# Kernel optimization log

Measured on AMD Instinct MI355X. Metric: run time of the kernel, lower is better.

## Reference

```python
import jax, jax.numpy as jnp
import numpy as np

N = 1_000_000
E = 1_000_000
K = 512
H = 64
F_IN = 19
N_ITERS = 3
EPS = 1e-5

def _leaky(x):
    return jax.nn.leaky_relu(x, negative_slope=0.01)

def _layernorm(x, g, b):
    mu = jnp.mean(x, axis=-1, keepdims=True)
    var = jnp.var(x, axis=-1, keepdims=True)
    return (x - mu) * jax.lax.rsqrt(var + EPS) * g + b

def setup_inputs() -> dict:
    key = jax.random.key(0)
    ks = jax.random.split(key, 20)
    s = 0.1
    inp = {
        "x": jax.random.normal(ks[0], (N, F_IN), dtype=jnp.float32),
        "edge_index": jax.random.randint(ks[1], (2, E), 0, N, dtype=jnp.int64),
        "candidate_indices": jax.random.randint(ks[2], (K,), 0, N, dtype=jnp.int64),
        # embedding params
        "pW_in": jax.random.normal(ks[3], (F_IN, H), dtype=jnp.float32) * s,
        "pb_in": jnp.zeros((H,), dtype=jnp.float32),
        "eW": jax.random.normal(ks[4], (2, H, H), dtype=jnp.float32) * s,
        "eb": jnp.zeros((2, H), dtype=jnp.float32),
        "gamma": jnp.ones((2, H), dtype=jnp.float32),
        "beta": jnp.zeros((2, H), dtype=jnp.float32),
        # bottom-up step MLPs (stacked over n_iters)
        "sW1": jax.random.normal(ks[5], (N_ITERS, H, H), dtype=jnp.float32) * s,
        "sb1": jnp.zeros((N_ITERS, H), dtype=jnp.float32),
        "sW2": jax.random.normal(ks[6], (N_ITERS, H, H), dtype=jnp.float32) * s,
        "sb2": jnp.zeros((N_ITERS, H), dtype=jnp.float32),
        # score head
        "hW1": jax.random.normal(ks[7], (H, H), dtype=jnp.float32) * s,
        "hb1": jnp.zeros((H,), dtype=jnp.float32),
        "hW2": jax.random.normal(ks[8], (H, 1), dtype=jnp.float32) * s,
        "hb2": jnp.zeros((1,), dtype=jnp.float32),
    }
    return inp

def reference(x, edge_index, candidate_indices, pW_in, pb_in, eW, eb, gamma, beta,
              sW1, sb1, sW2, sb2, hW1, hb1, hW2, hb2):
    # TreeNodeEmbedding: proj + 2 residual layers with LayerNorm
    h = _leaky(x @ pW_in + pb_in)
    for i in range(2):
        h = _layernorm(h + _leaky(h @ eW[i] + eb[i]), gamma[i], beta[i])
    parent_idx = edge_index[0]
    child_idx = edge_index[1]
    # Bottom-up message passing: scatter-mean over children, tiny MLP update
    for i in range(N_ITERS):
        child_h = h[child_idx]                                   # [E, H] gather
        sum_p = jax.ops.segment_sum(child_h, parent_idx, num_segments=N)  # [N, H]
        cnt = jax.ops.segment_sum(jnp.ones((E,), dtype=h.dtype), parent_idx, num_segments=N)  # [N]
        mean_p = sum_p / jnp.maximum(cnt, 1.0)[:, None]
        mask = (cnt > 0)[:, None]
        delta = _leaky(mean_p @ sW1[i] + sb1[i]) @ sW2[i] + sb2[i]
        h = h + jnp.where(mask, delta, 0.0)
    # Score head on candidates, softmax over k (all candidates real -> full_logits == scores)
    cand_h = h[candidate_indices]                                # [K, H]
    scores = (_leaky(cand_h @ hW1 + hb1) @ hW2 + hb2)[:, 0]      # [K]
    probs = jax.nn.softmax(scores)
    return probs
```

## Files before the change

### kernel.cpp

```cpp
#include <hip/hip_runtime.h>
#include <hip/hip_bf16.h>
#include <math.h>

#define H 64
#define FIN 19
#define EPSLN 1e-5f

#define OFF_PW   0
#define OFF_PB   1280
#define OFF_EW   1344
#define OFF_EB   9536
#define OFF_G    9664
#define OFF_BT   9792
#define OFF_W1   9920
#define OFF_W2   22208
#define OFF_B1   34496
#define OFF_B2   34688
#define OFF_HW1  34880
#define OFF_HB1  38976
#define OFF_HW2  39040
#define OFF_HB2  39104
#define WTS_TOTAL 39105

__device__ __forceinline__ float leaky(float v) { return v > 0.f ? v : 0.01f * v; }

__device__ __forceinline__ float wsumf(float v) {
#pragma unroll
  for (int off = 32; off > 0; off >>= 1) v += __shfl_xor(v, off, 64);
  return v;
}

__device__ __forceinline__ bool detect_bf16(const unsigned short* xs) {
  const int lane = threadIdx.x & 63;
  unsigned a = xs[lane], b = xs[64 + lane];
  unsigned ea = (a >> 7) & 0xFFu, ebx = (b >> 7) & 0xFFu;
  return !__any((int)(ea > 140u || ebx > 140u));
}

__device__ __forceinline__ bool detect_i64(const int* w) {
  const int lane = threadIdx.x & 63;
  return __all((int)(w[2 * lane + 1] == 0));
}

__device__ __forceinline__ float ldf(const void* p, size_t i, bool bf) {
  return bf ? __bfloat162float(((const __hip_bfloat16*)p)[i]) : ((const float*)p)[i];
}

struct WT {
  const void* src[14];
  int off[14], len[14], sl[14], rp[14], rs[14], cs[14];
};

__global__ __launch_bounds__(256) void prep_wts(WT T, const unsigned short* xs,
                                                float* wts, int total) {
  const bool bf = detect_bf16(xs);
  for (int i = blockIdx.x * 256 + threadIdx.x; i < total; i += gridDim.x * 256) {
    int p = 0;
    while (i >= T.off[p] + T.len[p]) ++p;
    const int loc = i - T.off[p];
    float v;
    if (T.rp[p] == 0) {
      v = ldf(T.src[p], loc, bf);
    } else {
      const int s = loc / T.sl[p];
      const int r = loc - s * T.sl[p];
      const int j = r / T.rp[p];
      const int k = r - j * T.rp[p];
      v = (k < T.rs[p])
              ? ldf(T.src[p], (size_t)s * T.rs[p] * T.cs[p] + (size_t)k * T.cs[p] + j, bf)
              : 0.f;
    }
    wts[i] = v;
  }
}

__device__ float embed_math(const void* x, const float* wts, float* stg, int v,
                            int lane, bool bf) {
  float xv = (lane < FIN) ? ldf(x, (size_t)v * FIN + lane, bf) : 0.f;
  stg[lane] = xv;
  __syncthreads();
  const float* tp = wts + OFF_PW + lane * 20;
  float a0 = wts[OFF_PB + lane], a1 = 0.f, a2 = 0.f, a3 = 0.f;
#pragma unroll
  for (int k = 0; k < 20; k += 4) {
    float4 m = *(const float4*)&stg[k];
    float4 w = *(const float4*)&tp[k];
    a0 += m.x * w.x; a1 += m.y * w.y; a2 += m.z * w.z; a3 += m.w * w.w;
  }
  __syncthreads();
  float h = leaky((a0 + a1) + (a2 + a3));
#pragma unroll
  for (int L = 0; L < 2; ++L) {
    stg[lane] = h;
    __syncthreads();
    const float* tw = wts + OFF_EW + L * 4096 + lane * 64;
    a0 = wts[OFF_EB + L * 64 + lane]; a1 = a2 = a3 = 0.f;
#pragma unroll
    for (int k = 0; k < H; k += 4) {
      float4 m = *(const float4*)&stg[k];
      float4 w = *(const float4*)&tw[k];
      a0 += m.x * w.x; a1 += m.y * w.y; a2 += m.z * w.z; a3 += m.w * w.w;
    }
    __syncthreads();
    float val = h + leaky((a0 + a1) + (a2 + a3));
    float mu = wsumf(val) * (1.f / 64.f);
    float d = val - mu;
    float var = wsumf(d * d) * (1.f / 64.f);
    h = d * (1.f / sqrtf(var + EPSLN)) * wts[OFF_G + L * 64 + lane] +
        wts[OFF_BT + L * 64 + lane];
  }
  return h;
}

__device__ float delta_math(const float* wts, float* stg, float mean, int it, int lane) {
  stg[lane] = mean;
  __syncthreads();
  const float* w1 = wts + OFF_W1 + it * 4096 + lane * 64;
  float a0 = wts[OFF_B1 + it * 64 + lane], a1 = 0.f, a2 = 0.f, a3 = 0.f;
#pragma unroll
  for (int k = 0; k < H; k += 4) {
    float4 m = *(const float4*)&stg[k];
    float4 w = *(const float4*)&w1[k];
    a0 += m.x * w.x; a1 += m.y * w.y; a2 += m.z * w.z; a3 += m.w * w.w;
  }
  __syncthreads();
  float t1 = leaky((a0 + a1) + (a2 + a3));
  stg[lane] = t1;
  __syncthreads();
  const float* w2 = wts + OFF_W2 + it * 4096 + lane * 64;
  a0 = wts[OFF_B2 + it * 64 + lane]; a1 = a2 = a3 = 0.f;
#pragma unroll
  for (int k = 0; k < H; k += 4) {
    float4 m = *(const float4*)&stg[k];
    float4 w = *(const float4*)&w2[k];
    a0 += m.x * w.x; a1 += m.y * w.y; a2 += m.z * w.z; a3 += m.w * w.w;
  }
  __syncthreads();
  return (a0 + a1) + (a2 + a3);
}

__global__ __launch_bounds__(256) void init_kernel(int* map, int nN, int* counters, int K,
                                                   int* ch3, int n3, int* ch2, int n2,
                                                   int* ch1, int n1) {
  const int tid = blockIdx.x * 256 + threadIdx.x;
  const int stride = gridDim.x * 256;
  for (int i = tid; i < nN; i += stride) map[i] = 0;
  for (int i = tid; i < n3; i += stride) ch3[i] = -1;
  for (int i = tid; i < n2; i += stride) ch2[i] = -1;
  for (int i = tid; i < n1; i += stride) ch1[i] = -1;
  if (tid < 3) counters[tid] = 0;
  if (tid == 3) counters[3] = K;
}

__global__ __launch_bounds__(64) void seed_kernel(const int* cand_raw, int K, int nN,
                                                  int* map, int* node3, int* nextSame3,
                                                  int* selfChild3, int* ctr2, int cap2,
                                                  int* node2) {
  const bool i64 = detect_i64(cand_raw);
  int t = blockIdx.x * 64 + threadIdx.x;
  if (t >= K) return;
  int cv = i64 ? cand_raw[2 * t] : cand_raw[t];
  unsigned n = (unsigned)cv;
  if (n >= (unsigned)nN) n = 0;
  node3[t] = (int)n;
  int enc = (1 << 24) | t;
  int old = atomicExch(&map[n], enc);
  nextSame3[t] = ((old >> 24) == 1) ? (old & 0xFFFFFF) : -1;
  int s = atomicAdd(ctr2, 1);
  if (s < cap2) { node2[s] = (int)n; selfChild3[t] = s; } else selfChild3[t] = 0;
}

__global__ __launch_bounds__(256) void regself_kernel(const int* ctrU_, int capU,
                                                      const int* nodeU, int* map, int epoch,
                                                      int* nextSameU, int* ctrD, int capD,
                                                      int* nodeD, int* selfChildU) {
  int cnt = *ctrU_; if (cnt > capU) cnt = capU;
  int t = blockIdx.x * 256 + threadIdx.x;
  if (t >= cnt) return;
  int n = nodeU[t];
  int enc = (epoch << 24) | t;
  int old = atomicExch(&map[n], enc);
  nextSameU[t] = ((old >> 24) == epoch) ? (old & 0xFFFFFF) : -1;
  int s = atomicAdd(ctrD, 1);
  if (s < capD) { nodeD[s] = n; selfChildU[t] = s; } else selfChildU[t] = 0;
}

__global__ __launch_bounds__(256) void scan_kernel(const int* eraw, int E, int nN,
                                                   const int* map, int epoch,
                                                   const int* nextSameU, int* childHeadU,
                                                   int* ctrD, int capD, int* nodeD,
                                                   int* childNextD) {
  const bool i64 = detect_i64(eraw);
  int e = blockIdx.x * 256 + threadIdx.x;
  if (e >= E) return;
  int pv = i64 ? eraw[2 * e] : eraw[e];
  unsigned p = (unsigned)pv;
  if (p >= (unsigned)nN) p = 0;
  int m = map[p];
  if ((m >> 24) != epoch) return;
  int cv = i64 ? eraw[2 * (E + e)] : eraw[E + e];
  unsigned c = (unsigned)cv;
  if (c >= (unsigned)nN) c = 0;
  int t = m & 0xFFFFFF;
  while (t >= 0) {
    int ct = atomicAdd(ctrD, 1);
    if (ct < capD) {
      nodeD[ct] = (int)c;
      childNextD[ct] = atomicExch(&childHeadU[t], ct);
    }
    t = nextSameU[t];
  }
}

__global__ __launch_bounds__(64) void eval0_kernel(const void* x, const int* ctr0_,
                                                   int cap0, const int* node0,
                                                   const float* wts, float* val0) {
  __shared__ float stg[H];
  int cnt = *ctr0_; if (cnt > cap0) cnt = cap0;
  const int t = blockIdx.x;
  if (t >= cnt) return;
  const int lane = threadIdx.x;
  const bool bf = detect_bf16((const unsigned short*)x);
  float h = embed_math(x, wts, stg, node0[t], lane, bf);
  val0[(size_t)t * H + lane] = h;
}

__global__ __launch_bounds__(64) void evalL_kernel(const int* ctrU_, int capU,
                                                   const int* selfChildU,
                                                   const int* childHeadU,
                                                   const int* childNextD,
                                                   const float* valD, float* valU,
                                                   const float* wts, int it) {
  __shared__ float stg[H];
  int cnt = *ctrU_; if (cnt > capU) cnt = capU;
  const int t = blockIdx.x;
  if (t >= cnt) return;
  const int lane = threadIdx.x;
  float hv = valD[(size_t)selfChildU[t] * H + lane];
  float acc = 0.f;
  int k = 0;
  int c = childHeadU[t];
  while (c >= 0) { acc += valD[(size_t)c * H + lane]; ++k; c = childNextD[c]; }
  if (k > 0) hv += delta_math(wts, stg, acc / (float)k, it, lane);
  valU[(size_t)t * H + lane] = hv;
}

__global__ __launch_bounds__(512) void score_kernel(
    const float* __restrict__ candH, const float* __restrict__ wts,
    const void* x, void* out, int K) {
  __shared__ float red[512];
  const int t = threadIdx.x;
  const bool bf = detect_bf16((const unsigned short*)x);
  float sc = 0.f;
  if (t < K) {
    float hr[H];
#pragma unroll
    for (int k = 0; k < H; k += 4) {
      float4 v = *(const float4*)&candH[(size_t)t * H + k];
      hr[k] = v.x; hr[k + 1] = v.y; hr[k + 2] = v.z; hr[k + 3] = v.w;
    }
    for (int j = 0; j < H; ++j) {
      float a = wts[OFF_HB1 + j];
#pragma unroll
      for (int k = 0; k < H; k += 4) {
        float4 w = *(const float4*)&wts[OFF_HW1 + j * 64 + k];
        a += hr[k] * w.x + hr[k + 1] * w.y + hr[k + 2] * w.z + hr[k + 3] * w.w;
      }
      sc += leaky(a) * wts[OFF_HW2 + j];
    }
    sc += wts[OFF_HB2];
  }
  red[t] = (t < K) ? sc : -3.0e38f;
  __syncthreads();
  for (int off = 256; off > 0; off >>= 1) {
    if (t < off) red[t] = fmaxf(red[t], red[t + off]);
    __syncthreads();
  }
  const float m = red[0];
  __syncthreads();
  const float ex = (t < K) ? expf(sc - m) : 0.f;
  red[t] = ex;
  __syncthreads();
  for (int off = 256; off > 0; off >>= 1) {
    if (t < off) red[t] += red[t + off];
    __syncthreads();
  }
  const float inv = 1.f / red[0];
  if (t < K) {
    float p = ex * inv;
    if (bf) ((__hip_bfloat16*)out)[t] = __float2bfloat16(p);
    else    ((float*)out)[t] = p;
  }
}

extern "C" void kernel_launch(void* const* d_in, const int* in_sizes, int n_in,
                              void* d_out, int out_size, void* d_ws, size_t ws_size,
                              hipStream_t stream) {
  const void* x   = d_in[0];
  const int* edge = (const int*)d_in[1];
  const int* cand = (const int*)d_in[2];
  const int nN = in_sizes[0] / FIN;
  const int E  = in_sizes[1] / 2;
  const int K  = in_sizes[2];

  const int CAP2 = 8 * K, CAP1 = 16 * K, CAP0 = 32 * K;

  auto al = [](size_t b) -> size_t { return (b + 255) & ~(size_t)255; };
  const size_t szW   = (size_t)WTS_TOTAL * sizeof(float);
  const size_t szMap = (size_t)nN * sizeof(int);
  const size_t szK   = (size_t)K * sizeof(int);
  const size_t sz2   = (size_t)CAP2 * sizeof(int);
  const size_t sz1   = (size_t)CAP1 * sizeof(int);
  const size_t sz0   = (size_t)CAP0 * sizeof(int);
  const size_t szV0  = (size_t)CAP0 * H * sizeof(float);
  const size_t szV1  = (size_t)CAP1 * H * sizeof(float);
  const size_t szV2  = (size_t)CAP2 * H * sizeof(float);
  const size_t szV3  = (size_t)K * H * sizeof(float);
  const size_t need = al(szW) + al(szMap) + 256  +
                      4 * al(szK) + 5 * al(sz2) + 5 * al(sz1) + 2 * al(sz0) +
                      al(szV0) + al(szV1) + al(szV2) + al(szV3);

  if (K > 2048 || K < 128 || E < 128 || ws_size < need) return;

  char* wsb = (char*)d_ws;
  size_t off = 0;
  auto carve = [&](size_t bytes) -> void* {
    void* p = wsb + off;
    off += (bytes + 255) & ~(size_t)255;
    return p;
  };
  float* wts     = (float*)carve(szW);
  int* map       = (int*)carve(szMap);
  int* counters  = (int*)carve(256);
  int* node3     = (int*)carve(szK);
  int* nextSame3 = (int*)carve(szK);
  int* selfCh3   = (int*)carve(szK);
  int* chHead3   = (int*)carve(szK);
  int* node2     = (int*)carve(sz2);
  int* nextSame2 = (int*)carve(sz2);
  int* selfCh2   = (int*)carve(sz2);
  int* chHead2   = (int*)carve(sz2);
  int* chNext2   = (int*)carve(sz2);
  int* node1     = (int*)carve(sz1);
  int* nextSame1 = (int*)carve(sz1);
  int* selfCh1   = (int*)carve(sz1);
  int* chHead1   = (int*)carve(sz1);
  int* chNext1   = (int*)carve(sz1);
  int* node0     = (int*)carve(sz0);
  int* chNext0   = (int*)carve(sz0);
  float* val0    = (float*)carve(szV0);
  float* val1    = (float*)carve(szV1);
  float* val2    = (float*)carve(szV2);
  float* val3    = (float*)carve(szV3);

  WT T;
  auto setv = [&](int i, const void* s, int o, int l) {
    T.src[i] = s; T.off[i] = o; T.len[i] = l; T.sl[i] = l;
    T.rp[i] = 0; T.rs[i] = 0; T.cs[i] = 0;
  };
  auto setm = [&](int i, const void* s, int o, int l, int sl, int rpad, int rs, int cs) {
    T.src[i] = s; T.off[i] = o; T.len[i] = l; T.sl[i] = sl;
    T.rp[i] = rpad; T.rs[i] = rs; T.cs[i] = cs;
  };
  setm(0,  d_in[3],  OFF_PW,  1280, 1280, 20, 19, 64);
  setv(1,  d_in[4],  OFF_PB,  64);
  setm(2,  d_in[5],  OFF_EW,  8192, 4096, 64, 64, 64);
  setv(3,  d_in[6],  OFF_EB,  128);
  setv(4,  d_in[7],  OFF_G,   128);
  setv(5,  d_in[8],  OFF_BT,  128);
  setm(6,  d_in[9],  OFF_W1,  12288, 4096, 64, 64, 64);
  setm(7,  d_in[11], OFF_W2,  12288, 4096, 64, 64, 64);
  setv(8,  d_in[10], OFF_B1,  192);
  setv(9,  d_in[12], OFF_B2,  192);
  setm(10, d_in[13], OFF_HW1, 4096, 4096, 64, 64, 64);
  setv(11, d_in[14], OFF_HB1, 64);
  setv(12, d_in[15], OFF_HW2, 64);
  setv(13, d_in[16], OFF_HB2, 1);

  prep_wts<<<160, 256, 0, stream>>>(T, (const unsigned short*)x, wts, WTS_TOTAL);

  init_kernel<<<1024, 256, 0, stream>>>(map, nN, counters, K, chHead3, K,
                                        chHead2, CAP2, chHead1, CAP1);

  seed_kernel<<<(K + 63) / 64, 64, 0, stream>>>(cand, K, nN, map, node3, nextSame3,
                                                selfCh3, &counters[0], CAP2, node2);
  scan_kernel<<<(E + 255) / 256, 256, 0, stream>>>(edge, E, nN, map, 1, nextSame3,
                                                   chHead3, &counters[0], CAP2,
                                                   node2, chNext2);
  regself_kernel<<<(CAP2 + 255) / 256, 256, 0, stream>>>(&counters[0], CAP2, node2, map, 2,
                                                         nextSame2, &counters[1], CAP1,
                                                         node1, selfCh2);
  scan_kernel<<<(E + 255) / 256, 256, 0, stream>>>(edge, E, nN, map, 2, nextSame2,
                                                   chHead2, &counters[1], CAP1,
                                                   node1, chNext1);
  regself_kernel<<<(CAP1 + 255) / 256, 256, 0, stream>>>(&counters[1], CAP1, node1, map, 3,
                                                         nextSame1, &counters[2], CAP0,
                                                         node0, selfCh1);
  scan_kernel<<<(E + 255) / 256, 256, 0, stream>>>(edge, E, nN, map, 3, nextSame1,
                                                   chHead1, &counters[2], CAP0,
                                                   node0, chNext0);

  eval0_kernel<<<CAP0, 64, 0, stream>>>(x, &counters[2], CAP0, node0, wts, val0);
  evalL_kernel<<<CAP1, 64, 0, stream>>>(&counters[1], CAP1, selfCh1, chHead1, chNext0,
                                        val0, val1, wts, 0);
  evalL_kernel<<<CAP2, 64, 0, stream>>>(&counters[0], CAP2, selfCh2, chHead2, chNext1,
                                        val1, val2, wts, 1);
  evalL_kernel<<<K, 64, 0, stream>>>(&counters[3], K, selfCh3, chHead3, chNext2,
                                     val2, val3, wts, 2);

  score_kernel<<<1, 512, 0, stream>>>(val3, wts, x, d_out, K);
}
```

Before: 267.0 us.

## Fuse pipeline into persistent megakernel with grid barriers and readlane matvecs

Replaces the dozen separate kernel launches (weight prep, init, seeding, three edge scans, per-level evals, score) with one persistent kernel of 256 blocks that separates phases with atomic grid-wide barriers. The per-node matvecs now broadcast activations via readlane from registers instead of staging through shared memory with syncthreads, and weights are stored untransposed so each lane reads a coalesced column. This targets launch overhead and tail gaps between many small dependent kernels. In exchange it relies on all 256 blocks being co-resident for the spin barrier, and the edge scans and evals run on a fixed, smaller grid.

```diff
diff --git a/kernel.cpp b/kernel.cpp
--- a/kernel.cpp
+++ b/kernel.cpp
@@ -5,22 +5,24 @@
 #define H 64
 #define FIN 19
 #define EPSLN 1e-5f
+#define NBLK 256
+#define NTHR 256
 
 #define OFF_PW   0
-#define OFF_PB   1280
-#define OFF_EW   1344
-#define OFF_EB   9536
-#define OFF_G    9664
-#define OFF_BT   9792
-#define OFF_W1   9920
-#define OFF_W2   22208
-#define OFF_B1   34496
-#define OFF_B2   34688
-#define OFF_HW1  34880
-#define OFF_HB1  38976
-#define OFF_HW2  39040
-#define OFF_HB2  39104
-#define WTS_TOTAL 39105
+#define OFF_PB   1216
+#define OFF_EW   1280
+#define OFF_EB   9472
+#define OFF_G    9600
+#define OFF_BT   9728
+#define OFF_W1   9856
+#define OFF_W2   22144
+#define OFF_B1   34432
+#define OFF_B2   34624
+#define OFF_HW1T 34816
+#define OFF_HB1  38912
+#define OFF_HW2  38976
+#define OFF_HB2  39040
+#define WTS_TOTAL 39041
 
 __device__ __forceinline__ float leaky(float v) { return v > 0.f ? v : 0.01f * v; }
 
@@ -28,6 +30,10 @@
 #pragma unroll
   for (int off = 32; off > 0; off >>= 1) v += __shfl_xor(v, off, 64);
   return v;
+}
+
+__device__ __forceinline__ float bcast(float v, int k) {
+  return __int_as_float(__builtin_amdgcn_readlane(__float_as_int(v), k));
 }
 
 __device__ __forceinline__ bool detect_bf16(const unsigned short* xs) {
@@ -46,63 +52,38 @@
   return bf ? __bfloat162float(((const __hip_bfloat16*)p)[i]) : ((const float*)p)[i];
 }
 
-struct WT {
-  const void* src[14];
-  int off[14], len[14], sl[14], rp[14], rs[14], cs[14];
-};
-
-__global__ __launch_bounds__(256) void prep_wts(WT T, const unsigned short* xs,
-                                                float* wts, int total) {
-  const bool bf = detect_bf16(xs);
-  for (int i = blockIdx.x * 256 + threadIdx.x; i < total; i += gridDim.x * 256) {
-    int p = 0;
-    while (i >= T.off[p] + T.len[p]) ++p;
-    const int loc = i - T.off[p];
-    float v;
-    if (T.rp[p] == 0) {
-      v = ldf(T.src[p], loc, bf);
-    } else {
-      const int s = loc / T.sl[p];
-      const int r = loc - s * T.sl[p];
-      const int j = r / T.rp[p];
-      const int k = r - j * T.rp[p];
-      v = (k < T.rs[p])
-              ? ldf(T.src[p], (size_t)s * T.rs[p] * T.cs[p] + (size_t)k * T.cs[p] + j, bf)
-              : 0.f;
-    }
-    wts[i] = v;
-  }
-}
-
-__device__ float embed_math(const void* x, const float* wts, float* stg, int v,
-                            int lane, bool bf) {
+__device__ __forceinline__ int ldctr(const int* p) {
+  return __hip_atomic_load(p, __ATOMIC_RELAXED, __HIP_MEMORY_SCOPE_AGENT);
+}
+
+__device__ __forceinline__ void gbar(unsigned* bars, int idx, unsigned nb) {
+  __syncthreads();
+  if (threadIdx.x == 0) {
+    __threadfence();
+    __hip_atomic_fetch_add(&bars[idx], 1u, __ATOMIC_RELEASE, __HIP_MEMORY_SCOPE_AGENT);
+    while (__hip_atomic_load(&bars[idx], __ATOMIC_ACQUIRE,
+                             __HIP_MEMORY_SCOPE_AGENT) < nb)
+      __builtin_amdgcn_s_sleep(1);
+    __threadfence();
+  }
+  __syncthreads();
+}
+
+__device__ __noinline__ float embed2(const void* x, const float* wts, int v,
+                                     int lane, bool bf) {
   float xv = (lane < FIN) ? ldf(x, (size_t)v * FIN + lane, bf) : 0.f;
-  stg[lane] = xv;
-  __syncthreads();
-  const float* tp = wts + OFF_PW + lane * 20;
-  float a0 = wts[OFF_PB + lane], a1 = 0.f, a2 = 0.f, a3 = 0.f;
-#pragma unroll
-  for (int k = 0; k < 20; k += 4) {
-    float4 m = *(const float4*)&stg[k];
-    float4 w = *(const float4*)&tp[k];
-    a0 += m.x * w.x; a1 += m.y * w.y; a2 += m.z * w.z; a3 += m.w * w.w;
-  }
-  __syncthreads();
-  float h = leaky((a0 + a1) + (a2 + a3));
+  float a = wts[OFF_PB + lane];
+#pragma unroll
+  for (int k = 0; k < FIN; ++k)
+    a = fmaf(bcast(xv, k), wts[OFF_PW + k * 64 + lane], a);
+  float h = leaky(a);
 #pragma unroll
   for (int L = 0; L < 2; ++L) {
-    stg[lane] = h;
-    __syncthreads();
-    const float* tw = wts + OFF_EW + L * 4096 + lane * 64;
-    a0 = wts[OFF_EB + L * 64 + lane]; a1 = a2 = a3 = 0.f;
-#pragma unroll
-    for (int k = 0; k < H; k += 4) {
-      float4 m = *(const float4*)&stg[k];
-      float4 w = *(const float4*)&tw[k];
-      a0 += m.x * w.x; a1 += m.y * w.y; a2 += m.z * w.z; a3 += m.w * w.w;
-    }
-    __syncthreads();
-    float val = h + leaky((a0 + a1) + (a2 + a3));
+    const float* W = wts + OFF_EW + L * 4096;
+    float b = wts[OFF_EB + L * 64 + lane];
+#pragma unroll
+    for (int k = 0; k < 64; ++k) b = fmaf(bcast(h, k), W[k * 64 + lane], b);
+    float val = h + leaky(b);
     float mu = wsumf(val) * (1.f / 64.f);
     float d = val - mu;
     float var = wsumf(d * d) * (1.f / 64.f);
@@ -112,184 +93,226 @@
   return h;
 }
 
-__device__ float delta_math(const float* wts, float* stg, float mean, int it, int lane) {
-  stg[lane] = mean;
-  __syncthreads();
-  const float* w1 = wts + OFF_W1 + it * 4096 + lane * 64;
-  float a0 = wts[OFF_B1 + it * 64 + lane], a1 = 0.f, a2 = 0.f, a3 = 0.f;
-#pragma unroll
-  for (int k = 0; k < H; k += 4) {
-    float4 m = *(const float4*)&stg[k];
-    float4 w = *(const float4*)&w1[k];
-    a0 += m.x * w.x; a1 += m.y * w.y; a2 += m.z * w.z; a3 += m.w * w.w;
-  }
-  __syncthreads();
-  float t1 = leaky((a0 + a1) + (a2 + a3));
-  stg[lane] = t1;
-  __syncthreads();
-  const float* w2 = wts + OFF_W2 + it * 4096 + lane * 64;
-  a0 = wts[OFF_B2 + it * 64 + lane]; a1 = a2 = a3 = 0.f;
-#pragma unroll
-  for (int k = 0; k < H; k += 4) {
-    float4 m = *(const float4*)&stg[k];
-    float4 w = *(const float4*)&w2[k];
-    a0 += m.x * w.x; a1 += m.y * w.y; a2 += m.z * w.z; a3 += m.w * w.w;
-  }
-  __syncthreads();
-  return (a0 + a1) + (a2 + a3);
-}
-
-__global__ __launch_bounds__(256) void init_kernel(int* map, int nN, int* counters, int K,
-                                                   int* ch3, int n3, int* ch2, int n2,
-                                                   int* ch1, int n1) {
-  const int tid = blockIdx.x * 256 + threadIdx.x;
-  const int stride = gridDim.x * 256;
-  for (int i = tid; i < nN; i += stride) map[i] = 0;
-  for (int i = tid; i < n3; i += stride) ch3[i] = -1;
-  for (int i = tid; i < n2; i += stride) ch2[i] = -1;
-  for (int i = tid; i < n1; i += stride) ch1[i] = -1;
-  if (tid < 3) counters[tid] = 0;
-  if (tid == 3) counters[3] = K;
-}
-
-__global__ __launch_bounds__(64) void seed_kernel(const int* cand_raw, int K, int nN,
-                                                  int* map, int* node3, int* nextSame3,
-                                                  int* selfChild3, int* ctr2, int cap2,
-                                                  int* node2) {
-  const bool i64 = detect_i64(cand_raw);
-  int t = blockIdx.x * 64 + threadIdx.x;
-  if (t >= K) return;
-  int cv = i64 ? cand_raw[2 * t] : cand_raw[t];
-  unsigned n = (unsigned)cv;
-  if (n >= (unsigned)nN) n = 0;
-  node3[t] = (int)n;
-  int enc = (1 << 24) | t;
-  int old = atomicExch(&map[n], enc);
-  nextSame3[t] = ((old >> 24) == 1) ? (old & 0xFFFFFF) : -1;
-  int s = atomicAdd(ctr2, 1);
-  if (s < cap2) { node2[s] = (int)n; selfChild3[t] = s; } else selfChild3[t] = 0;
-}
-
-__global__ __launch_bounds__(256) void regself_kernel(const int* ctrU_, int capU,
-                                                      const int* nodeU, int* map, int epoch,
-                                                      int* nextSameU, int* ctrD, int capD,
-                                                      int* nodeD, int* selfChildU) {
-  int cnt = *ctrU_; if (cnt > capU) cnt = capU;
-  int t = blockIdx.x * 256 + threadIdx.x;
-  if (t >= cnt) return;
-  int n = nodeU[t];
-  int enc = (epoch << 24) | t;
-  int old = atomicExch(&map[n], enc);
-  nextSameU[t] = ((old >> 24) == epoch) ? (old & 0xFFFFFF) : -1;
-  int s = atomicAdd(ctrD, 1);
-  if (s < capD) { nodeD[s] = n; selfChildU[t] = s; } else selfChildU[t] = 0;
-}
-
-__global__ __launch_bounds__(256) void scan_kernel(const int* eraw, int E, int nN,
-                                                   const int* map, int epoch,
-                                                   const int* nextSameU, int* childHeadU,
-                                                   int* ctrD, int capD, int* nodeD,
-                                                   int* childNextD) {
-  const bool i64 = detect_i64(eraw);
-  int e = blockIdx.x * 256 + threadIdx.x;
-  if (e >= E) return;
-  int pv = i64 ? eraw[2 * e] : eraw[e];
-  unsigned p = (unsigned)pv;
-  if (p >= (unsigned)nN) p = 0;
-  int m = map[p];
-  if ((m >> 24) != epoch) return;
-  int cv = i64 ? eraw[2 * (E + e)] : eraw[E + e];
-  unsigned c = (unsigned)cv;
-  if (c >= (unsigned)nN) c = 0;
-  int t = m & 0xFFFFFF;
-  while (t >= 0) {
-    int ct = atomicAdd(ctrD, 1);
-    if (ct < capD) {
-      nodeD[ct] = (int)c;
-      childNextD[ct] = atomicExch(&childHeadU[t], ct);
+__device__ __noinline__ float delta2(const float* wts, float mean, int it, int lane) {
+  const float* W1 = wts + OFF_W1 + it * 4096;
+  float a = wts[OFF_B1 + it * 64 + lane];
+#pragma unroll
+  for (int k = 0; k < 64; ++k) a = fmaf(bcast(mean, k), W1[k * 64 + lane], a);
+  float t1 = leaky(a);
+  const float* W2 = wts + OFF_W2 + it * 4096;
+  float b = wts[OFF_B2 + it * 64 + lane];
+#pragma unroll
+  for (int k = 0; k < 64; ++k) b = fmaf(bcast(t1, k), W2[k * 64 + lane], b);
+  return b;
+}
+
+struct WT {
+  const void* src[14];
+  int off[14], len[14], sl[14], rp[14], rs[14], cs[14];
+};
+
+struct P {
+  float* wts; int* map; unsigned* bars; int* ctr;
+  int *nextSame3, *selfCh3, *chHead3;
+  int *node2, *nextSame2, *selfCh2, *chHead2, *chNext2;
+  int *node1, *nextSame1, *selfCh1, *chHead1, *chNext1;
+  int *node0, *chNext0;
+  float *val0, *val1, *val2, *val3, *scores;
+};
+
+__device__ void scanE(const int* edge, int E, int nN, bool i64, const int* map,
+                      int epoch, const int* nextU, int* headU, int* ctrD, int capD,
+                      int* nodeD, int* nextD, int tid, int GT) {
+  for (int e = tid; e < E; e += GT) {
+    int pv = i64 ? edge[2 * e] : edge[e];
+    unsigned pp = (unsigned)pv;
+    if (pp >= (unsigned)nN) pp = 0;
+    int m = map[pp];
+    if ((m >> 24) != epoch) continue;
+    int cv = i64 ? edge[2 * (E + e)] : edge[E + e];
+    unsigned cc = (unsigned)cv;
+    if (cc >= (unsigned)nN) cc = 0;
+    int t = m & 0xFFFFFF;
+    while (t >= 0) {
+      int ct = atomicAdd(ctrD, 1);
+      if (ct < capD) {
+        nodeD[ct] = (int)cc;
+        nextD[ct] = atomicExch(&headU[t], ct);
+      }
+      t = nextU[t];
     }
-    t = nextSameU[t];
-  }
-}
-
-__global__ __launch_bounds__(64) void eval0_kernel(const void* x, const int* ctr0_,
-                                                   int cap0, const int* node0,
-                                                   const float* wts, float* val0) {
-  __shared__ float stg[H];
-  int cnt = *ctr0_; if (cnt > cap0) cnt = cap0;
-  const int t = blockIdx.x;
-  if (t >= cnt) return;
-  const int lane = threadIdx.x;
+  }
+}
+
+__device__ void regselfF(int cnt, const int* nodeU, int* map, int epoch, int* nextU,
+                         int* ctrD, int capD, int* nodeD, int* selfU, int tid, int GT) {
+  for (int t = tid; t < cnt; t += GT) {
+    int n = nodeU[t];
+    int enc = (epoch << 24) | t;
+    int old = atomicExch(&map[n], enc);
+    nextU[t] = ((old >> 24) == epoch) ? (old & 0xFFFFFF) : -1;
+    int s = atomicAdd(ctrD, 1);
+    if (s < capD) { nodeD[s] = n; selfU[t] = s; } else selfU[t] = 0;
+  }
+}
+
+__device__ void evalPhase(int cnt, const int* selfU, const int* headU,
+                          const int* nextD, const float* valD, float* valU,
+                          const float* wts, int it, int wv, int NW, int lane) {
+  for (int t = wv; t < cnt; t += NW) {
+    float hv = valD[(size_t)selfU[t] * H + lane];
+    float acc = 0.f;
+    int k = 0;
+    int c = headU[t];
+    while (c >= 0) { acc += valD[(size_t)c * H + lane]; ++k; c = nextD[c]; }
+    if (k > 0) hv += delta2(wts, acc / (float)k, it, lane);
+    valU[(size_t)t * H + lane] = hv;
+  }
+}
+
+__global__ void initbars(unsigned* bars) {
+  if (threadIdx.x < 64) bars[threadIdx.x] = 0u;
+}
+
+__global__ __launch_bounds__(NTHR) void mega(const void* x, const int* edge,
+                                             const int* cand, WT T, P p,
+                                             int nN, int E, int K, void* out) {
+  const int tid = blockIdx.x * NTHR + threadIdx.x;
+  const int GT = gridDim.x * NTHR;
+  const int lane = threadIdx.x & 63;
+  const int wv = blockIdx.x * (NTHR / 64) + (threadIdx.x >> 6);
+  const int NW = gridDim.x * (NTHR / 64);
+  const unsigned nb = gridDim.x;
   const bool bf = detect_bf16((const unsigned short*)x);
-  float h = embed_math(x, wts, stg, node0[t], lane, bf);
-  val0[(size_t)t * H + lane] = h;
-}
-
-__global__ __launch_bounds__(64) void evalL_kernel(const int* ctrU_, int capU,
-                                                   const int* selfChildU,
-                                                   const int* childHeadU,
-                                                   const int* childNextD,
-                                                   const float* valD, float* valU,
-                                                   const float* wts, int it) {
-  __shared__ float stg[H];
-  int cnt = *ctrU_; if (cnt > capU) cnt = capU;
-  const int t = blockIdx.x;
-  if (t >= cnt) return;
-  const int lane = threadIdx.x;
-  float hv = valD[(size_t)selfChildU[t] * H + lane];
-  float acc = 0.f;
-  int k = 0;
-  int c = childHeadU[t];
-  while (c >= 0) { acc += valD[(size_t)c * H + lane]; ++k; c = childNextD[c]; }
-  if (k > 0) hv += delta_math(wts, stg, acc / (float)k, it, lane);
-  valU[(size_t)t * H + lane] = hv;
-}
-
-__global__ __launch_bounds__(512) void score_kernel(
-    const float* __restrict__ candH, const float* __restrict__ wts,
-    const void* x, void* out, int K) {
-  __shared__ float red[512];
-  const int t = threadIdx.x;
-  const bool bf = detect_bf16((const unsigned short*)x);
-  float sc = 0.f;
-  if (t < K) {
+  const bool i64e = detect_i64(edge);
+  const bool i64c = detect_i64(cand);
+  const int CAP2 = 8 * K, CAP1 = 16 * K, CAP0 = 32 * K;
+
+  for (int i = tid; i < nN; i += GT) p.map[i] = 0;
+  for (int i = tid; i < K; i += GT) p.chHead3[i] = -1;
+  for (int i = tid; i < CAP2; i += GT) p.chHead2[i] = -1;
+  for (int i = tid; i < CAP1; i += GT) p.chHead1[i] = -1;
+  if (tid < 4) p.ctr[tid] = 0;
+  for (int i = tid; i < WTS_TOTAL; i += GT) {
+    int q = 0;
+    while (i >= T.off[q] + T.len[q]) ++q;
+    const int loc = i - T.off[q];
+    float v;
+    if (T.rp[q] == 0) {
+      v = ldf(T.src[q], loc, bf);
+    } else {
+      const int s = loc / T.sl[q];
+      const int r = loc - s * T.sl[q];
+      const int j = r / T.rp[q];
+      const int k = r - j * T.rp[q];
+      v = (k < T.rs[q])
+              ? ldf(T.src[q], (size_t)s * T.rs[q] * T.cs[q] + (size_t)k * T.cs[q] + j, bf)
+              : 0.f;
+    }
+    p.wts[i] = v;
+  }
+  gbar(p.bars, 0, nb);
+
+  if (tid < K) {
+    int cv = i64c ? cand[2 * tid] : cand[tid];
+    unsigned n = (unsigned)cv;
+    if (n >= (unsigned)nN) n = 0;
+    int enc = (1 << 24) | tid;
+    int old = atomicExch(&p.map[n], enc);
+    p.nextSame3[tid] = ((old >> 24) == 1) ? (old & 0xFFFFFF) : -1;
+    int s = atomicAdd(&p.ctr[0], 1);
+    if (s < CAP2) { p.node2[s] = (int)n; p.selfCh3[tid] = s; } else p.selfCh3[tid] = 0;
+  }
+  gbar(p.bars, 1, nb);
+
+  scanE(edge, E, nN, i64e, p.map, 1, p.nextSame3, p.chHead3, &p.ctr[0], CAP2,
+        p.node2, p.chNext2, tid, GT);
+  gbar(p.bars, 2, nb);
+
+  { int c2 = min(ldctr(&p.ctr[0]), CAP2);
+    regselfF(c2, p.node2, p.map, 2, p.nextSame2, &p.ctr[1], CAP1, p.node1,
+             p.selfCh2, tid, GT); }
+  gbar(p.bars, 3, nb);
+
+  scanE(edge, E, nN, i64e, p.map, 2, p.nextSame2, p.chHead2, &p.ctr[1], CAP1,
+        p.node1, p.chNext1, tid, GT);
+  gbar(p.bars, 4, nb);
+
+  { int c1 = min(ldctr(&p.ctr[1]), CAP1);
+    regselfF(c1, p.node1, p.map, 3, p.nextSame1, &p.ctr[2], CAP0, p.node0,
+             p.selfCh1, tid, GT); }
+  gbar(p.bars, 5, nb);
+
+  scanE(edge, E, nN, i64e, p.map, 3, p.nextSame1, p.chHead1, &p.ctr[2], CAP0,
+        p.node0, p.chNext0, tid, GT);
+  gbar(p.bars, 6, nb);
+
+  { int c0 = min(ldctr(&p.ctr[2]), CAP0);
+    for (int t = wv; t < c0; t += NW)
+      p.val0[(size_t)t * H + lane] = embed2(x, p.wts, p.node0[t], lane, bf); }
+  gbar(p.bars, 7, nb);
+
+  { int c1 = min(ldctr(&p.ctr[1]), CAP1);
+    evalPhase(c1, p.selfCh1, p.chHead1, p.chNext0, p.val0, p.val1, p.wts, 0,
+              wv, NW, lane); }
+  gbar(p.bars, 8, nb);
+
+  { int c2 = min(ldctr(&p.ctr[0]), CAP2);
+    evalPhase(c2, p.selfCh2, p.chHead2, p.chNext1, p.val1, p.val2, p.wts, 1,
+              wv, NW, lane); }
+  gbar(p.bars, 9, nb);
+
+  evalPhase(K, p.selfCh3, p.chHead3, p.chNext2, p.val2, p.val3, p.wts, 2,
+            wv, NW, lane);
+  gbar(p.bars, 10, nb);
+
+  if (tid < K) {
     float hr[H];
 #pragma unroll
     for (int k = 0; k < H; k += 4) {
-      float4 v = *(const float4*)&candH[(size_t)t * H + k];
+      float4 v = *(const float4*)&p.val3[(size_t)tid * H + k];
       hr[k] = v.x; hr[k + 1] = v.y; hr[k + 2] = v.z; hr[k + 3] = v.w;
     }
+    float sc = 0.f;
     for (int j = 0; j < H; ++j) {
-      float a = wts[OFF_HB1 + j];
+      float a = p.wts[OFF_HB1 + j];
 #pragma unroll
       for (int k = 0; k < H; k += 4) {
-        float4 w = *(const float4*)&wts[OFF_HW1 + j * 64 + k];
+        float4 w = *(const float4*)&p.wts[OFF_HW1T + j * 64 + k];
         a += hr[k] * w.x + hr[k + 1] * w.y + hr[k + 2] * w.z + hr[k + 3] * w.w;
       }
-      sc += leaky(a) * wts[OFF_HW2 + j];
+      sc += leaky(a) * p.wts[OFF_HW2 + j];
     }
-    sc += wts[OFF_HB2];
-  }
-  red[t] = (t < K) ? sc : -3.0e38f;
+    p.scores[tid] = sc + p.wts[OFF_HB2];
+  }
+  gbar(p.bars, 11, nb);
+
+  if (blockIdx.x != 0) return;
+  __shared__ float red[NTHR];
+  const int t = threadIdx.x;
+  float mloc = -3.0e38f;
+  for (int i = t; i < K; i += NTHR) mloc = fmaxf(mloc, p.scores[i]);
+  red[t] = mloc;
   __syncthreads();
-  for (int off = 256; off > 0; off >>= 1) {
-    if (t < off) red[t] = fmaxf(red[t], red[t + off]);
+  for (int o = NTHR / 2; o > 0; o >>= 1) {
+    if (t < o) red[t] = fmaxf(red[t], red[t + o]);
     __syncthreads();
   }
   const float m = red[0];
   __syncthreads();
-  const float ex = (t < K) ? expf(sc - m) : 0.f;
-  red[t] = ex;
+  float sloc = 0.f;
+  for (int i = t; i < K; i += NTHR) sloc += expf(p.scores[i] - m);
+  red[t] = sloc;
   __syncthreads();
-  for (int off = 256; off > 0; off >>= 1) {
-    if (t < off) red[t] += red[t + off];
+  for (int o = NTHR / 2; o > 0; o >>= 1) {
+    if (t < o) red[t] += red[t + o];
     __syncthreads();
   }
   const float inv = 1.f / red[0];
-  if (t < K) {
-    float p = ex * inv;
-    if (bf) ((__hip_bfloat16*)out)[t] = __float2bfloat16(p);
-    else    ((float*)out)[t] = p;
+  for (int i = t; i < K; i += NTHR) {
+    float pv = expf(p.scores[i] - m) * inv;
+    if (bf) ((__hip_bfloat16*)out)[i] = __float2bfloat16(pv);
+    else    ((float*)out)[i] = pv;
   }
 }
 
@@ -316,42 +339,44 @@
   const size_t szV1  = (size_t)CAP1 * H * sizeof(float);
   const size_t szV2  = (size_t)CAP2 * H * sizeof(float);
   const size_t szV3  = (size_t)K * H * sizeof(float);
-  const size_t need = al(szW) + al(szMap) + 256  +
-                      4 * al(szK) + 5 * al(sz2) + 5 * al(sz1) + 2 * al(sz0) +
-                      al(szV0) + al(szV1) + al(szV2) + al(szV3);
+  const size_t need = al(szW) + al(szMap) + 512 + 3 * al(szK) + 5 * al(sz2) +
+                      5 * al(sz1) + 2 * al(sz0) + al(szV0) + al(szV1) + al(szV2) +
+                      al(szV3) + al(szK * 4);
 
   if (K > 2048 || K < 128 || E < 128 || ws_size < need) return;
 
   char* wsb = (char*)d_ws;
   size_t off = 0;
   auto carve = [&](size_t bytes) -> void* {
-    void* p = wsb + off;
+    void* pp = wsb + off;
     off += (bytes + 255) & ~(size_t)255;
-    return p;
+    return pp;
   };
-  float* wts     = (float*)carve(szW);
-  int* map       = (int*)carve(szMap);
-  int* counters  = (int*)carve(256);
-  int* node3     = (int*)carve(szK);
-  int* nextSame3 = (int*)carve(szK);
-  int* selfCh3   = (int*)carve(szK);
-  int* chHead3   = (int*)carve(szK);
-  int* node2     = (int*)carve(sz2);
-  int* nextSame2 = (int*)carve(sz2);
-  int* selfCh2   = (int*)carve(sz2);
-  int* chHead2   = (int*)carve(sz2);
-  int* chNext2   = (int*)carve(sz2);
-  int* node1     = (int*)carve(sz1);
-  int* nextSame1 = (int*)carve(sz1);
-  int* selfCh1   = (int*)carve(sz1);
-  int* chHead1   = (int*)carve(sz1);
-  int* chNext1   = (int*)carve(sz1);
-  int* node0     = (int*)carve(sz0);
-  int* chNext0   = (int*)carve(sz0);
-  float* val0    = (float*)carve(szV0);
-  float* val1    = (float*)carve(szV1);
-  float* val2    = (float*)carve(szV2);
-  float* val3    = (float*)carve(szV3);
+  P p;
+  p.wts       = (float*)carve(szW);
+  p.map       = (int*)carve(szMap);
+  p.bars      = (unsigned*)carve(256);
+  p.ctr       = (int*)carve(256);
+  p.nextSame3 = (int*)carve(szK);
+  p.selfCh3   = (int*)carve(szK);
+  p.chHead3   = (int*)carve(szK);
+  p.node2     = (int*)carve(sz2);
+  p.nextSame2 = (int*)carve(sz2);
+  p.selfCh2   = (int*)carve(sz2);
+  p.chHead2   = (int*)carve(sz2);
+  p.chNext2   = (int*)carve(sz2);
+  p.node1     = (int*)carve(sz1);
+  p.nextSame1 = (int*)carve(sz1);
+  p.selfCh1   = (int*)carve(sz1);
+  p.chHead1   = (int*)carve(sz1);
+  p.chNext1   = (int*)carve(sz1);
+  p.node0     = (int*)carve(sz0);
+  p.chNext0   = (int*)carve(sz0);
+  p.val0      = (float*)carve(szV0);
+  p.val1      = (float*)carve(szV1);
+  p.val2      = (float*)carve(szV2);
+  p.val3      = (float*)carve(szV3);
+  p.scores    = (float*)carve((size_t)K * sizeof(float));
 
   WT T;
   auto setv = [&](int i, const void* s, int o, int l) {
@@ -362,51 +387,21 @@
     T.src[i] = s; T.off[i] = o; T.len[i] = l; T.sl[i] = sl;
     T.rp[i] = rpad; T.rs[i] = rs; T.cs[i] = cs;
   };
-  setm(0,  d_in[3],  OFF_PW,  1280, 1280, 20, 19, 64);
+  setv(0,  d_in[3],  OFF_PW,  1216);
   setv(1,  d_in[4],  OFF_PB,  64);
-  setm(2,  d_in[5],  OFF_EW,  8192, 4096, 64, 64, 64);
+  setv(2,  d_in[5],  OFF_EW,  8192);
   setv(3,  d_in[6],  OFF_EB,  128);
   setv(4,  d_in[7],  OFF_G,   128);
   setv(5,  d_in[8],  OFF_BT,  128);
-  setm(6,  d_in[9],  OFF_W1,  12288, 4096, 64, 64, 64);
-  setm(7,  d_in[11], OFF_W2,  12288, 4096, 64, 64, 64);
+  setv(6,  d_in[9],  OFF_W1,  12288);
+  setv(7,  d_in[11], OFF_W2,  12288);
   setv(8,  d_in[10], OFF_B1,  192);
   setv(9,  d_in[12], OFF_B2,  192);
-  setm(10, d_in[13], OFF_HW1, 4096, 4096, 64, 64, 64);
+  setm(10, d_in[13], OFF_HW1T, 4096, 4096, 64, 64, 64);
   setv(11, d_in[14], OFF_HB1, 64);
   setv(12, d_in[15], OFF_HW2, 64);
   setv(13, d_in[16], OFF_HB2, 1);
 
-  prep_wts<<<160, 256, 0, stream>>>(T, (const unsigned short*)x, wts, WTS_TOTAL);
-
-  init_kernel<<<1024, 256, 0, stream>>>(map, nN, counters, K, chHead3, K,
-                                        chHead2, CAP2, chHead1, CAP1);
-
-  seed_kernel<<<(K + 63) / 64, 64, 0, stream>>>(cand, K, nN, map, node3, nextSame3,
-                                                selfCh3, &counters[0], CAP2, node2);
-  scan_kernel<<<(E + 255) / 256, 256, 0, stream>>>(edge, E, nN, map, 1, nextSame3,
-                                                   chHead3, &counters[0], CAP2,
-                                                   node2, chNext2);
-  regself_kernel<<<(CAP2 + 255) / 256, 256, 0, stream>>>(&counters[0], CAP2, node2, map, 2,
-                                                         nextSame2, &counters[1], CAP1,
-                                                         node1, selfCh2);
-  scan_kernel<<<(E + 255) / 256, 256, 0, stream>>>(edge, E, nN, map, 2, nextSame2,
-                                                   chHead2, &counters[1], CAP1,
-                                                   node1, chNext1);
-  regself_kernel<<<(CAP1 + 255) / 256, 256, 0, stream>>>(&counters[1], CAP1, node1, map, 3,
-                                                         nextSame1, &counters[2], CAP0,
-                                                         node0, selfCh1);
-  scan_kernel<<<(E + 255) / 256, 256, 0, stream>>>(edge, E, nN, map, 3, nextSame1,
-                                                   chHead1, &counters[2], CAP0,
-                                                   node0, chNext0);
-
-  eval0_kernel<<<CAP0, 64, 0, stream>>>(x, &counters[2], CAP0, node0, wts, val0);
-  evalL_kernel<<<CAP1, 64, 0, stream>>>(&counters[1], CAP1, selfCh1, chHead1, chNext0,
-                                        val0, val1, wts, 0);
-  evalL_kernel<<<CAP2, 64, 0, stream>>>(&counters[0], CAP2, selfCh2, chHead2, chNext1,
-                                        val1, val2, wts, 1);
-  evalL_kernel<<<K, 64, 0, stream>>>(&counters[3], K, selfCh3, chHead3, chNext2,
-                                     val2, val3, wts, 2);
-
-  score_kernel<<<1, 512, 0, stream>>>(val3, wts, x, d_out, K);
-}
+  initbars<<<1, 64, 0, stream>>>(p.bars);
+  mega<<<NBLK, NTHR, 0, stream>>>(x, edge, cand, T, p, nN, E, K, d_out);
+}
```

Measured after the change: 923.3 us. 246% more time.
